# Optimization experiments

Hardware: AMD Instinct MI355X
Metric: run time of the kernel (lower is better)

The kernel has to match this reference:

```python
import jax, jax.numpy as jnp
import numpy as np
import math

B, H, W, CIN = 8, 64, 64, 192
INNER, K, N, P = 384, 2, 32, 64
NHK = INNER // P          # heads per scan direction = 6
NH = K * NHK              # total heads = 12
HID = 4 * CIN

def _silu(v):
    return v * jax.nn.sigmoid(v)

def setup_inputs() -> dict:
    key = jax.random.key(0)
    ks = jax.random.split(key, 12)
    x = jax.random.normal(ks[0], (B, H, W, CIN), jnp.float32)
    W_in = jax.random.normal(ks[1], (2 * INNER, CIN), jnp.float32) * 0.02
    conv_w = jax.random.normal(ks[2], (INNER, 1, 3, 3), jnp.float32) * 0.1
    conv_b = jnp.zeros((INNER,), jnp.float32)
    x_proj_weight = jax.random.normal(ks[3], (K, 2 * N + NHK, INNER), jnp.float32) * 0.02
    A_logs = jnp.log(jax.random.uniform(ks[4], (NH,), jnp.float32, 1.0, 16.0))
    Ds = jnp.ones((NH,), jnp.float32)
    u = jax.random.uniform(ks[5], (NH,), jnp.float32)
    dt = jnp.exp(u * (math.log(0.1) - math.log(0.001)) + math.log(0.001))
    dt = jnp.clip(dt, 1e-4, None)
    dt_bias = dt + jnp.log(-jnp.expm1(-dt))
    init_states = jnp.zeros((NH, P, N), jnp.float32)
    W_out = jax.random.normal(ks[6], (CIN, INNER), jnp.float32) * 0.02
    W1 = jax.random.normal(ks[7], (HID, CIN), jnp.float32) * 0.02
    b1 = jnp.zeros((HID,), jnp.float32)
    W2 = jax.random.normal(ks[8], (CIN, HID), jnp.float32) * 0.02
    b2 = jnp.zeros((CIN,), jnp.float32)
    return dict(x=x, W_in=W_in, conv_w=conv_w, conv_b=conv_b, x_proj_weight=x_proj_weight,
                A_logs=A_logs, Ds=Ds, dt_bias=dt_bias, init_states=init_states,
                W_out=W_out, W1=W1, b1=b1, W2=W2, b2=b2)

def reference(x, W_in, conv_w, conv_b, x_proj_weight, A_logs, Ds, dt_bias,
              init_states, W_out, W1, b1, W2, b2):
    Bb, Hh, Ww, Cin = x.shape
    L = Hh * Ww
    inner = W_in.shape[0] // 2
    shortcut = x
    # norm1 is identity (norm=None). in_proj (no bias), split into x and gate z
    xz = jnp.einsum('bhwc,dc->bhwd', x, W_in)
    xl, z = jnp.split(xz, 2, axis=-1)
    # depthwise conv (NCHW) + SiLU
    xc = jnp.transpose(xl, (0, 3, 1, 2))
    xc = jax.lax.conv_general_dilated(xc, conv_w, (1, 1), 'SAME',
                                      feature_group_count=inner,
                                      dimension_numbers=('NCHW', 'OIHW', 'NCHW'))
    xc = _silu(xc + conv_b[None, :, None, None])
    # cross scan: row-major and transposed (W-major) flattenings
    xs = jnp.stack([xc.reshape(Bb, inner, L),
                    jnp.transpose(xc, (0, 1, 3, 2)).reshape(Bb, inner, L)], axis=1)  # (B,K,inner,L)
    # project to B, C, dt per direction
    BCdt = jnp.einsum('bkdl,kcd->blkc', xs, x_proj_weight)  # (B,L,K,2N+NHK)
    Bs = BCdt[..., :N]                     # (B,L,K,N)
    Cs = BCdt[..., N:2 * N]                # (B,L,K,N)
    dt = BCdt[..., 2 * N:].reshape(Bb, L, NH)
    xh = jnp.transpose(xs, (0, 3, 1, 2)).reshape(Bb, L, NH, P)  # heads: k-major
    # Mamba2 selective scan (dt_softplus with bias)
    dt = jax.nn.softplus(dt + dt_bias)     # (B,L,NH)
    A = -jnp.exp(A_logs)                   # (NH,)
    da = jnp.exp(dt * A)                   # (B,L,NH)
    dtx = dt[..., None] * xh               # (B,L,NH,P)
    Bh = jnp.repeat(Bs, NHK, axis=2)       # (B,L,NH,N) group -> heads
    Ch = jnp.repeat(Cs, NHK, axis=2)
    h0 = jnp.broadcast_to(init_states, (Bb,) + init_states.shape)  # (B,NH,P,N)
    def step(h, inp):
        da_t, dtx_t, B_t, C_t = inp
        h = da_t[..., None, None] * h + dtx_t[..., None] * B_t[:, :, None, :]
        y_t = jnp.einsum('bhpn,bhn->bhp', h, C_t)
        return h, y_t
    _, ys = jax.lax.scan(step, h0, (jnp.moveaxis(da, 1, 0), jnp.moveaxis(dtx, 1, 0),
                                    jnp.moveaxis(Bh, 1, 0), jnp.moveaxis(Ch, 1, 0)))
    y = jnp.moveaxis(ys, 0, 1) + Ds[None, None, :, None] * xh  # (B,L,NH,P)
    out_y = jnp.transpose(y.reshape(Bb, L, K, inner), (0, 2, 3, 1))  # (B,K,inner,L)
    # scan_proj: undo each direction's flattening and sum
    y0 = out_y[:, 0].reshape(Bb, inner, Hh, Ww)
    y1 = jnp.transpose(out_y[:, 1].reshape(Bb, inner, Ww, Hh), (0, 1, 3, 2))
    yr = jnp.transpose((y0 + y1).reshape(Bb, inner, L), (0, 2, 1)).reshape(Bb, Hh, Ww, inner)
    # gate, out_proj, residual, MLP branch (dense is identity since in==out)
    yg = yr * _silu(z)
    out = shortcut + jnp.einsum('bhwd,cd->bhwc', yg, W_out)
    h1 = _silu(jnp.einsum('...c,dc->...d', out, W1) + b1)
    mlp = jnp.einsum('...d,cd->...c', h1, W2) + b2
    return out + mlp
```

## Files before the change

### kernel.cpp

```cpp
#include <hip/hip_runtime.h>
#include <math.h>

#define BB 8
#define HH 64
#define WW 64
#define CIN 192
#define INNER 384
#define LL 4096
#define NSTATE 32
#define PDIM 64
#define NHK 6
#define NHEADS 12
#define HID 768
#define CPROJ 70
#define QC 64
#define NC 64

#define WS_XLZ   0u
#define WS_XC    50331648u
#define WS_Y1    75497472u
#define WS_BCBF  100663296u
#define WS_DTRAW 109051904u
#define WS_DTV   119013376u
#define WS_CUMS  120586240u
#define WS_SHB   122159104u
#define WS_Y0    147324928u
#define WS_XBF   172490752u
#define WS_WINB  185073664u
#define WS_WPADB 185368576u
#define WS_WOUTB 185565184u
#define WS_W1B   185761792u
#define WS_W2B   186056704u
#define WS_REQ   186449920u

typedef __attribute__((ext_vector_type(8))) short short8;
typedef __attribute__((ext_vector_type(4))) float f32x4;

__device__ __forceinline__ float silu_f(float x) { return x / (1.f + __expf(-x)); }

__device__ __forceinline__ unsigned short f2bf(float f) {
    unsigned u = __float_as_uint(f);
    u += 0x7fffu + ((u >> 16) & 1u);
    return (unsigned short)(u >> 16);
}
__device__ __forceinline__ float bf2f(unsigned short u) {
    return __uint_as_float(((unsigned)u) << 16);
}

template<int EPI, int TRANSA>
__global__ __launch_bounds__(256)
void gemm_bf16(const unsigned short* __restrict__ A, const unsigned short* __restrict__ Wt,
               const float* __restrict__ bias, const float* __restrict__ res,
               float* __restrict__ Cf, unsigned short* __restrict__ Cb,
               int Kd, int ldc, int nmax)
{
    __shared__ __align__(16) short Als[128 * 64];
    __shared__ __align__(16) short Bls[128 * 64];
    const int tid = threadIdx.x;
    const int m0 = blockIdx.x * 128;
    const int n0 = blockIdx.y * 128;
    const int lane = tid & 63;
    const int wv = tid >> 6;
    const int wm = (wv >> 1) << 6;
    const int wn = (wv & 1) << 6;

    const unsigned short* gA[4];
    const unsigned short* gB[4];
    int lw[4];
    #pragma unroll
    for (int c = 0; c < 4; ++c) {
        const int idx = c * 256 + tid;
        const int row = idx >> 3;
        const int kb  = idx & 7;
        const int sb  = kb ^ (row & 7);
        lw[c] = row * 64 + sb * 8;
        size_t arow;
        const int mm = m0 + row;
        if (TRANSA) {
            const int bq = mm >> 12, lq = mm & 4095;
            arow = ((size_t)bq << 12) + (size_t)(((lq & 63) << 6) + (lq >> 6));
        } else {
            arow = (size_t)mm;
        }
        gA[c] = A + arow * Kd + kb * 8;
        gB[c] = Wt + (size_t)(n0 + row) * Kd + kb * 8;
    }

    f32x4 acc[4][4];
    #pragma unroll
    for (int i = 0; i < 4; ++i)
        #pragma unroll
        for (int j = 0; j < 4; ++j) acc[i][j] = (f32x4){0.f, 0.f, 0.f, 0.f};

    const int NT = Kd >> 6;
    short8 pA[4], pB[4];
    #pragma unroll
    for (int c = 0; c < 4; ++c) {
        pA[c] = *(const short8*)(gA[c]);
        pB[c] = *(const short8*)(gB[c]);
    }
    for (int kt = 0; kt < NT; ++kt) {
        __syncthreads();
        #pragma unroll
        for (int c = 0; c < 4; ++c) {
            *(short8*)&Als[lw[c]] = pA[c];
            *(short8*)&Bls[lw[c]] = pB[c];
        }
        __syncthreads();
        if (kt + 1 < NT) {
            #pragma unroll
            for (int c = 0; c < 4; ++c) {
                pA[c] = *(const short8*)(gA[c] + (kt + 1) * 64);
                pB[c] = *(const short8*)(gB[c] + (kt + 1) * 64);
            }
        }
        #pragma unroll
        for (int ks = 0; ks < 2; ++ks) {
            short8 af[4], bfr[4];
            #pragma unroll
            for (int r = 0; r < 4; ++r) {
                const int rowa = wm + r * 16 + (lane & 15);
                const int rowb = wn + r * 16 + (lane & 15);
                const int kb = ks * 4 + (lane >> 4);
                af[r]  = *(const short8*)&Als[rowa * 64 + ((kb ^ (rowa & 7)) << 3)];
                bfr[r] = *(const short8*)&Bls[rowb * 64 + ((kb ^ (rowb & 7)) << 3)];
            }
            #pragma unroll
            for (int mr = 0; mr < 4; ++mr)
                #pragma unroll
                for (int nr = 0; nr < 4; ++nr)
                    acc[mr][nr] = __builtin_amdgcn_mfma_f32_16x16x32_bf16(af[mr], bfr[nr], acc[mr][nr], 0, 0, 0);
        }
    }
    #pragma unroll
    for (int mr = 0; mr < 4; ++mr) {
        #pragma unroll
        for (int nr = 0; nr < 4; ++nr) {
            const int n = n0 + wn + nr * 16 + (lane & 15);
            if (n >= nmax) continue;
            const int mb = m0 + wm + mr * 16 + ((lane >> 4) << 2);
            #pragma unroll
            for (int q = 0; q < 4; ++q) {
                const size_t off = (size_t)(mb + q) * ldc + n;
                float v = acc[mr][nr][q];
                if (EPI == 0) { Cf[off] = v; }
                else if (EPI == 1) { v = silu_f(v + bias[n]); Cb[off] = f2bf(v); }
                else if (EPI == 2) { v += bias[n] + res[off]; Cf[off] = v; }
                else if (EPI == 3) { v += res[off]; Cf[off] = v; Cb[off] = f2bf(v); }
                else if (EPI == 4) { Cb[off] = f2bf(v); }
                else if (EPI == 5) {
                    if (n < 64) Cb[(size_t)(mb + q) * 128 + n] = f2bf(v);
                    else        Cf[(size_t)(mb + q) * 12 + (n - 64)] = v;
                }
            }
        }
    }
}

__global__ __launch_bounds__(256)
void cvt_kernel(const float* __restrict__ src, unsigned short* __restrict__ dst, int n)
{
    const int i = blockIdx.x * 256 + threadIdx.x;
    if (i < n) dst[i] = f2bf(src[i]);
}

__global__ __launch_bounds__(256)
void cvt_pad_kernel(const float* __restrict__ src, unsigned short* __restrict__ dst,
                    int srcRows, int total, int cols)
{
    const int i = blockIdx.x * 256 + threadIdx.x;
    if (i >= total) return;
    const int r = i / cols;
    dst[i] = (r < srcRows) ? f2bf(src[i]) : (unsigned short)0;
}

__global__ __launch_bounds__(256)
void conv_dw_kernel(const unsigned short* __restrict__ xlz, const float* __restrict__ cw,
                    const float* __restrict__ cb, unsigned short* __restrict__ xcbf)
{
    const int t = blockIdx.x * 256 + threadIdx.x;
    const int dv = t % (INNER / 8);
    const int m  = t / (INNER / 8);
    const int b = m >> 12;
    const int r = m & 4095;
    const int i = r >> 6;
    const int j = r & 63;
    const int d0 = dv * 8;

    float wreg[72];
    {
        const float4* w4 = (const float4*)(cw + d0 * 9);
        #pragma unroll
        for (int u = 0; u < 18; ++u) {
            const float4 v = w4[u];
            wreg[4*u+0] = v.x; wreg[4*u+1] = v.y; wreg[4*u+2] = v.z; wreg[4*u+3] = v.w;
        }
    }
    float acc[8];
    {
        const float4 b0 = *(const float4*)(cb + d0);
        const float4 b1 = *(const float4*)(cb + d0 + 4);
        acc[0]=b0.x; acc[1]=b0.y; acc[2]=b0.z; acc[3]=b0.w;
        acc[4]=b1.x; acc[5]=b1.y; acc[6]=b1.z; acc[7]=b1.w;
    }
    #pragma unroll
    for (int di = 0; di < 3; ++di) {
        const int ii = i + di - 1;
        if (ii < 0 || ii >= HH) continue;
        #pragma unroll
        for (int dj = 0; dj < 3; ++dj) {
            const int jj = j + dj - 1;
            if (jj < 0 || jj >= WW) continue;
            const uint4 v = *(const uint4*)(xlz + (((size_t)b << 12) + (size_t)(ii * 64 + jj)) * 768 + d0);
            const int t9 = di * 3 + dj;
            const unsigned ua[4] = {v.x, v.y, v.z, v.w};
            #pragma unroll
            for (int w2 = 0; w2 < 4; ++w2) {
                const float xlo = __uint_as_float(ua[w2] << 16);
                const float xhi = __uint_as_float(ua[w2] & 0xffff0000u);
                acc[2*w2+0] = fmaf(xlo, wreg[(2*w2+0)*9 + t9], acc[2*w2+0]);
                acc[2*w2+1] = fmaf(xhi, wreg[(2*w2+1)*9 + t9], acc[2*w2+1]);
            }
        }
    }
    unsigned o[4];
    #pragma unroll
    for (int w2 = 0; w2 < 4; ++w2) {
        const unsigned lo = f2bf(silu_f(acc[2*w2+0]));
        const unsigned hi = f2bf(silu_f(acc[2*w2+1]));
        o[w2] = lo | (hi << 16);
    }
    *(uint4*)(xcbf + (size_t)m * INNER + d0) = make_uint4(o[0], o[1], o[2], o[3]);
}

__global__ __launch_bounds__(256)
void dtcums_kernel(const float* __restrict__ dtraw, const float* __restrict__ dt_bias,
                   const float* __restrict__ A_logs,
                   float* __restrict__ dtv, float* __restrict__ cums)
{
    const int w = blockIdx.x * 4 + (threadIdx.x >> 6);
    const int lane = threadIdx.x & 63;
    const int b = w / (NHEADS * NC);
    const int rem = w - b * (NHEADS * NC);
    const int h = rem / NC;
    const int c = rem - h * NC;
    const int k = h / NHK;
    const int hq = h - k * NHK;
    const int l = c * QC + lane;
    const float dtr = dtraw[(((size_t)b * LL + l) * 2 + k) * 6 + hq];
    const float xx = dtr + dt_bias[h];
    const float sp = (xx > 20.f) ? xx : log1pf(expf(xx));
    float s = -expf(A_logs[h]) * sp;
    #pragma unroll
    for (int d = 1; d < 64; d <<= 1) {
        const float o = __shfl_up(s, d);
        if (lane >= d) s += o;
    }
    dtv[((size_t)b * LL + l) * NHEADS + h] = sp;
    cums[((size_t)b * LL + l) * NHEADS + h] = s;
}

__global__ __launch_bounds__(256)
void chunk_state_kernel(const unsigned short* __restrict__ xcbf, const unsigned short* __restrict__ BCbf,
                        const float* __restrict__ dtv, const float* __restrict__ cums,
                        unsigned short* __restrict__ SHb)
{
    __shared__ __align__(16) unsigned short Xb[PDIM][72];
    __shared__ __align__(16) unsigned short Bsc[NSTATE][72];
    __shared__ float cuS[QC], rs[QC];
    const int c = blockIdx.x, h = blockIdx.y, b = blockIdx.z;
    const int k = h / NHK;
    const int dch0 = (h - k * NHK) * PDIM;
    const int tid = threadIdx.x;
    const int lane = tid & 63;
    const int w = tid >> 6;

    #pragma unroll
    for (int r = 0; r < 16; ++r) {
        const int idx = tid + r * 256;
        const int m = idx >> 6, p = idx & 63;
        const int pos = (k == 0) ? (c * QC + m) : (m * QC + c);
        Xb[p][m] = xcbf[(((size_t)b << 12) + pos) * INNER + dch0 + p];
    }
    if (tid < QC)
        cuS[tid] = cums[((size_t)b * LL + c * QC + tid) * NHEADS + h];
    __syncthreads();
    if (tid < QC)
        rs[tid] = dtv[((size_t)b * LL + c * QC + tid) * NHEADS + h] * __expf(cuS[QC-1] - cuS[tid]);
    __syncthreads();
    #pragma unroll
    for (int r = 0; r < 8; ++r) {
        const int idx = tid + r * 256;
        const int m = idx >> 5, n = idx & 31;
        Bsc[n][m] = f2bf(rs[m] * bf2f(BCbf[(((size_t)b * LL + c * QC + m) * 2 + k) * 64 + n]));
    }
    __syncthreads();

    const int rowf = lane & 15;
    const int ko   = lane >> 4;
    f32x4 acc[2] = {{0.f,0.f,0.f,0.f},{0.f,0.f,0.f,0.f}};
    #pragma unroll
    for (int ks = 0; ks < 2; ++ks) {
        const short8 af = *(const short8*)&Xb[w * 16 + rowf][ks * 32 + ko * 8];
        #pragma unroll
        for (int nt = 0; nt < 2; ++nt) {
            const short8 bfr = *(const short8*)&Bsc[nt * 16 + rowf][ks * 32 + ko * 8];
            acc[nt] = __builtin_amdgcn_mfma_f32_16x16x32_bf16(af, bfr, acc[nt], 0, 0, 0);
        }
    }
    unsigned short* base = SHb + ((((size_t)b * NHEADS + h) * NC + c) * PDIM) * NSTATE;
    #pragma unroll
    for (int nt = 0; nt < 2; ++nt) {
        #pragma unroll
        for (int q = 0; q < 4; ++q) {
            const int p = w * 16 + ko * 4 + q;
            base[p * NSTATE + nt * 16 + rowf] = f2bf(acc[nt][q]);
        }
    }
}

__global__ __launch_bounds__(64)
void state_scan_kernel(unsigned short* __restrict__ SHb, const float* __restrict__ cums,
                       const float* __restrict__ init_states)
{
    __shared__ float decays[NC];
    const int g = blockIdx.x;
    const int bh = g >> 2;
    const int quarter = g & 3;
    const int b = bh / NHEADS;
    const int h = bh % NHEADS;
    const int tid = threadIdx.x;
    decays[tid] = __expf(cums[((size_t)b * LL + tid * QC + QC - 1) * NHEADS + h]);
    __syncthreads();
    const int p = quarter * 16 + (tid >> 2);
    const int nb = (tid & 3) * 8;
    float hs[8];
    {
        const float* is = init_states + ((size_t)h * PDIM + p) * NSTATE + nb;
        #pragma unroll
        for (int i = 0; i < 8; ++i) hs[i] = is[i];
    }
    unsigned short* base = SHb + (((size_t)b * NHEADS + h) * NC) * (PDIM * NSTATE) + p * NSTATE + nb;
    for (int c = 0; c < NC; ++c) {
        unsigned short* slot = base + (size_t)c * (PDIM * NSTATE);
        const uint4 sv = *(const uint4*)slot;
        const unsigned ua[4] = {sv.x, sv.y, sv.z, sv.w};
        unsigned o[4];
        #pragma unroll
        for (int w2 = 0; w2 < 4; ++w2)
            o[w2] = (unsigned)f2bf(hs[2*w2]) | ((unsigned)f2bf(hs[2*w2+1]) << 16);
        *(uint4*)slot = make_uint4(o[0], o[1], o[2], o[3]);
        const float dc = decays[c];
        #pragma unroll
        for (int w2 = 0; w2 < 4; ++w2) {
            hs[2*w2+0] = fmaf(dc, hs[2*w2+0], __uint_as_float(ua[w2] << 16));
            hs[2*w2+1] = fmaf(dc, hs[2*w2+1], __uint_as_float(ua[w2] & 0xffff0000u));
        }
    }
}

__global__ __launch_bounds__(256)
void intra_kernel(const unsigned short* __restrict__ xcbf, const unsigned short* __restrict__ BCbf,
                  const float* __restrict__ dtv, const float* __restrict__ cums,
                  const unsigned short* __restrict__ SHb, const float* __restrict__ Ds,
                  unsigned short* __restrict__ y0, unsigned short* __restrict__ y1)
{
    __shared__ __align__(16) unsigned short Bs[QC][40];
    __shared__ __align__(16) unsigned short Cs[QC][40];
    __shared__ __align__(16) unsigned short Hs[PDIM][40];
    __shared__ __align__(16) unsigned short Xb[PDIM][72];
    __shared__ __align__(16) unsigned short Gb[QC][72];
    __shared__ float cuS[QC], dtS[QC], Ei[QC];
    const int c = blockIdx.x, h = blockIdx.y, b = blockIdx.z;
    const int k = h / NHK;
    const int dch0 = (h - k * NHK) * PDIM;
    const int tid = threadIdx.x;
    const int lane = tid & 63;
    const int w = tid >> 6;

    #pragma unroll
    for (int r = 0; r < 16; ++r) {
        const int idx = tid + r * 256;
        const int m = idx >> 6, p = idx & 63;
        const int pos = (k == 0) ? (c * QC + m) : (m * QC + c);
        Xb[p][m] = xcbf[(((size_t)b << 12) + pos) * INNER + dch0 + p];
    }
    #pragma unroll
    for (int r = 0; r < 2; ++r) {
        const int idx = tid + r * 256;
        const int i = idx >> 3, ch = idx & 7;
        const uint4 v = *(const uint4*)(BCbf + (((size_t)b * LL + c * QC + i) * 2 + k) * 64 + ch * 8);
        if (ch < 4) *(uint4*)&Bs[i][ch * 8] = v;
        else        *(uint4*)&Cs[i][(ch - 4) * 8] = v;
    }
    {
        const int p = tid >> 2, ch = tid & 3;
        *(uint4*)&Hs[p][ch * 8] =
            *(const uint4*)(SHb + ((((size_t)b * NHEADS + h) * NC + c) * PDIM + p) * NSTATE + ch * 8);
    }
    if (tid < QC) {
        const size_t o = ((size_t)b * LL + c * QC + tid) * NHEADS + h;
        const float cu = cums[o];
        cuS[tid] = cu;
        dtS[tid] = dtv[o];
        Ei[tid]  = __expf(cu);
    }
    __syncthreads();

    const int rowf = lane & 15;
    const int ko   = lane >> 4;
    const short8 cfrag = *(const short8*)&Cs[w * 16 + rowf][ko * 8];

    f32x4 graw[4];
    #pragma unroll
    for (int mt = 0; mt < 4; ++mt) {
        const short8 bfrag = *(const short8*)&Bs[mt * 16 + rowf][ko * 8];
        graw[mt] = __builtin_amdgcn_mfma_f32_16x16x32_bf16(cfrag, bfrag, (f32x4){0.f,0.f,0.f,0.f}, 0, 0, 0);
    }
    #pragma unroll
    for (int mt = 0; mt < 4; ++mt) {
        const int m = mt * 16 + rowf;
        const float cum = cuS[m];
        const float dtm = dtS[m];
        #pragma unroll
        for (int q = 0; q < 4; ++q) {
            const int i = w * 16 + ko * 4 + q;
            float g = 0.f;
            if (m <= i) g = __expf(fminf(cuS[i] - cum, 0.f)) * dtm * graw[mt][q];
            Gb[i][m] = f2bf(g);
        }
    }
    f32x4 acc[4];
    #pragma unroll
    for (int pt = 0; pt < 4; ++pt) {
        const short8 hfrag = *(const short8*)&Hs[pt * 16 + rowf][ko * 8];
        acc[pt] = __builtin_amdgcn_mfma_f32_16x16x32_bf16(cfrag, hfrag, (f32x4){0.f,0.f,0.f,0.f}, 0, 0, 0);
    }
    const float Dh = Ds[h];
    #pragma unroll
    for (int pt = 0; pt < 4; ++pt) {
        const int p = pt * 16 + rowf;
        #pragma unroll
        for (int q = 0; q < 4; ++q) {
            const int i = w * 16 + ko * 4 + q;
            acc[pt][q] = acc[pt][q] * Ei[i] + Dh * bf2f(Xb[p][i]);
        }
    }
    #pragma unroll
    for (int ks = 0; ks < 2; ++ks) {
        const short8 gfrag = *(const short8*)&Gb[w * 16 + rowf][ks * 32 + ko * 8];
        #pragma unroll
        for (int pt = 0; pt < 4; ++pt) {
            const short8 xfrag = *(const short8*)&Xb[pt * 16 + rowf][ks * 32 + ko * 8];
            acc[pt] = __builtin_amdgcn_mfma_f32_16x16x32_bf16(gfrag, xfrag, acc[pt], 0, 0, 0);
        }
    }
    unsigned short* yk = (k == 0) ? y0 : y1;
    #pragma unroll
    for (int pt = 0; pt < 4; ++pt) {
        const int p = pt * 16 + rowf;
        #pragma unroll
        for (int q = 0; q < 4; ++q) {
            const int i = w * 16 + ko * 4 + q;
            const int pos = (k == 0) ? (c * QC + i) : (i * QC + c);
            yk[(((size_t)b << 12) + pos) * INNER + dch0 + p] = f2bf(acc[pt][q]);
        }
    }
}

__global__ __launch_bounds__(256)
void gate_kernel(const unsigned short* __restrict__ y0, const unsigned short* __restrict__ y1,
                 const unsigned short* __restrict__ xlz, unsigned short* __restrict__ ygbf)
{
    const int t = blockIdx.x * 256 + threadIdx.x;
    const int dv = t % (INNER / 8);
    const int m  = t / (INNER / 8);
    const int d0 = dv * 8;
    const uint4 a = *(const uint4*)(y0 + (size_t)m * INNER + d0);
    const uint4 bv = *(const uint4*)(y1 + (size_t)m * INNER + d0);
    const uint4 zv = *(const uint4*)(xlz + (size_t)m * 768 + INNER + d0);
    const unsigned ua[4] = {a.x, a.y, a.z, a.w};
    const unsigned ub[4] = {bv.x, bv.y, bv.z, bv.w};
    const unsigned uz[4] = {zv.x, zv.y, zv.z, zv.w};
    unsigned o[4];
    #pragma unroll
    for (int w2 = 0; w2 < 4; ++w2) {
        const float ylo = __uint_as_float(ua[w2] << 16) + __uint_as_float(ub[w2] << 16);
        const float yhi = __uint_as_float(ua[w2] & 0xffff0000u) + __uint_as_float(ub[w2] & 0xffff0000u);
        const float zlo = __uint_as_float(uz[w2] << 16);
        const float zhi = __uint_as_float(uz[w2] & 0xffff0000u);
        o[w2] = (unsigned)f2bf(ylo * silu_f(zlo)) | ((unsigned)f2bf(yhi * silu_f(zhi)) << 16);
    }
    *(uint4*)(ygbf + (size_t)m * INNER + d0) = make_uint4(o[0], o[1], o[2], o[3]);
}

__global__ __launch_bounds__(256)
void report_ws_kernel(float* __restrict__ out, int n, float val)
{
    const int e = blockIdx.x * 256 + threadIdx.x;
    if (e < n) out[e] = val;
}

extern "C" void kernel_launch(void* const* d_in, const int* in_sizes, int n_in,
                              void* d_out, int out_size, void* d_ws, size_t ws_size,
                              hipStream_t stream)
{
    const float* x          = (const float*)d_in[0];
    const float* W_in       = (const float*)d_in[1];
    const float* conv_w     = (const float*)d_in[2];
    const float* conv_b     = (const float*)d_in[3];
    const float* xpw        = (const float*)d_in[4];
    const float* A_logs     = (const float*)d_in[5];
    const float* Ds         = (const float*)d_in[6];
    const float* dt_bias    = (const float*)d_in[7];
    const float* init_states= (const float*)d_in[8];
    const float* W_out      = (const float*)d_in[9];
    const float* W1         = (const float*)d_in[10];
    const float* b1         = (const float*)d_in[11];
    const float* W2         = (const float*)d_in[12];
    const float* b2         = (const float*)d_in[13];
    float* out = (float*)d_out;

    if (ws_size < (size_t)WS_REQ) {
        const float mib = (float)((double)ws_size / 1048576.0);
        report_ws_kernel<<<(out_size + 255) / 256, 256, 0, stream>>>(out, out_size, mib);
        return;
    }

    char* ws = (char*)d_ws;
    unsigned short* xlz   = (unsigned short*)(ws + WS_XLZ);
    unsigned short* xc_bf = (unsigned short*)(ws + WS_XC);
    unsigned short* y1    = (unsigned short*)(ws + WS_Y1);
    unsigned short* BCbf  = (unsigned short*)(ws + WS_BCBF);
    float* dtraw = (float*)(ws + WS_DTRAW);
    float* dtv   = (float*)(ws + WS_DTV);
    float* cums  = (float*)(ws + WS_CUMS);
    unsigned short* SHb   = (unsigned short*)(ws + WS_SHB);
    unsigned short* y0    = (unsigned short*)(ws + WS_Y0);
    unsigned short* x_bf  = (unsigned short*)(ws + WS_XBF);
    unsigned short* Winb  = (unsigned short*)(ws + WS_WINB);
    unsigned short* wpadb = (unsigned short*)(ws + WS_WPADB);
    unsigned short* Woutb = (unsigned short*)(ws + WS_WOUTB);
    unsigned short* W1b   = (unsigned short*)(ws + WS_W1B);
    unsigned short* W2b   = (unsigned short*)(ws + WS_W2B);
    unsigned short* yg_bf  = (unsigned short*)(ws + WS_XC);
    unsigned short* out_bf = (unsigned short*)(ws + WS_BCBF);
    unsigned short* h1_bf  = (unsigned short*)(ws + WS_XLZ);

    const int M = BB * LL;

    cvt_kernel<<<(M * CIN + 255) / 256, 256, 0, stream>>>(x, x_bf, M * CIN);
    cvt_kernel<<<(HID * CIN + 255) / 256, 256, 0, stream>>>(W_in, Winb, HID * CIN);
    cvt_kernel<<<(HID * CIN + 255) / 256, 256, 0, stream>>>(W1, W1b, HID * CIN);
    cvt_pad_kernel<<<(128 * INNER + 255) / 256, 256, 0, stream>>>(xpw, wpadb, CPROJ, 128 * INNER, INNER);
    cvt_pad_kernel<<<(128 * INNER + 255) / 256, 256, 0, stream>>>(xpw + CPROJ * INNER, wpadb + 128 * INNER, CPROJ, 128 * INNER, INNER);
    cvt_pad_kernel<<<(256 * INNER + 255) / 256, 256, 0, stream>>>(W_out, Woutb, CIN, 256 * INNER, INNER);
    cvt_pad_kernel<<<(256 * HID + 255) / 256, 256, 0, stream>>>(W2, W2b, CIN, 256 * HID, HID);

    gemm_bf16<4,0><<<dim3(M/128, HID/128), 256, 0, stream>>>(x_bf, Winb, nullptr, nullptr, nullptr, xlz, CIN, HID, HID);

    conv_dw_kernel<<<(M * INNER / 8) / 256, 256, 0, stream>>>(xlz, conv_w, conv_b, xc_bf);

    gemm_bf16<5,0><<<dim3(M/128, 1), 256, 0, stream>>>(xc_bf, wpadb, nullptr, nullptr, dtraw, BCbf, INNER, 0, CPROJ);
    gemm_bf16<5,1><<<dim3(M/128, 1), 256, 0, stream>>>(xc_bf, wpadb + 128 * INNER, nullptr, nullptr, dtraw + 6, BCbf + 64, INNER, 0, CPROJ);

    dtcums_kernel<<<(BB * NHEADS * NC) / 4, 256, 0, stream>>>(dtraw, dt_bias, A_logs, dtv, cums);

    chunk_state_kernel<<<dim3(NC, NHEADS, BB), 256, 0, stream>>>(xc_bf, BCbf, dtv, cums, SHb);
    state_scan_kernel<<<BB * NHEADS * 4, 64, 0, stream>>>(SHb, cums, init_states);
    intra_kernel<<<dim3(NC, NHEADS, BB), 256, 0, stream>>>(xc_bf, BCbf, dtv, cums, SHb, Ds, y0, y1);

    gate_kernel<<<(M * INNER / 8) / 256, 256, 0, stream>>>(y0, y1, xlz, yg_bf);

    gemm_bf16<3,0><<<dim3(M/128, 2), 256, 0, stream>>>(yg_bf, Woutb, nullptr, x, out, out_bf, INNER, CIN, CIN);

    gemm_bf16<1,0><<<dim3(M/128, HID/128), 256, 0, stream>>>(out_bf, W1b, b1, nullptr, nullptr, h1_bf, CIN, HID, HID);
    gemm_bf16<2,0><<<dim3(M/128, 2), 256, 0, stream>>>(h1_bf, W2b, b2, out, out, nullptr, HID, CIN, CIN);
}
```

Baseline: 275.9 us.

## Merge weight conversions into one kernel and reuse rows in depthwise conv

Six separate weight-conversion launches are replaced by a single kernel that branches on flat index, cutting launch overhead. The depthwise 3x3 conv now has each thread compute 8 vertically consecutive output pixels, keeping a sliding window of three input rows in registers. Each new output row then needs 3 loads instead of 9. The trade-offs are higher register pressure and 8x fewer threads, which lowers available parallelism.

```diff
diff --git a/kernel.cpp b/kernel.cpp
--- a/kernel.cpp
+++ b/kernel.cpp
@@ -165,13 +165,36 @@
 }
 
 __global__ __launch_bounds__(256)
-void cvt_pad_kernel(const float* __restrict__ src, unsigned short* __restrict__ dst,
-                    int srcRows, int total, int cols)
-{
-    const int i = blockIdx.x * 256 + threadIdx.x;
-    if (i >= total) return;
-    const int r = i / cols;
-    dst[i] = (r < srcRows) ? f2bf(src[i]) : (unsigned short)0;
+void cvt_weights_kernel(const float* __restrict__ W_in, const float* __restrict__ W1,
+                        const float* __restrict__ xpw, const float* __restrict__ W_out,
+                        const float* __restrict__ W2,
+                        unsigned short* __restrict__ Winb, unsigned short* __restrict__ W1b,
+                        unsigned short* __restrict__ wpadb, unsigned short* __restrict__ Woutb,
+                        unsigned short* __restrict__ W2b)
+{
+    int i = blockIdx.x * 256 + threadIdx.x;
+    if (i < 147456) { Winb[i] = f2bf(W_in[i]); return; }
+    i -= 147456;
+    if (i < 147456) { W1b[i] = f2bf(W1[i]); return; }
+    i -= 147456;
+    if (i < 98304) {
+        const int d = i % 384;
+        const int rr = (i / 384) & 127;
+        const int k = i / 49152;
+        wpadb[i] = (rr < CPROJ) ? f2bf(xpw[((size_t)k * CPROJ + rr) * 384 + d]) : (unsigned short)0;
+        return;
+    }
+    i -= 98304;
+    if (i < 98304) {
+        const int rr = i / 384;
+        Woutb[i] = (rr < CIN) ? f2bf(W_out[i]) : (unsigned short)0;
+        return;
+    }
+    i -= 98304;
+    if (i < 196608) {
+        const int rr = i / 768;
+        W2b[i] = (rr < CIN) ? f2bf(W2[i]) : (unsigned short)0;
+    }
 }
 
 __global__ __launch_bounds__(256)
@@ -179,13 +202,13 @@
                     const float* __restrict__ cb, unsigned short* __restrict__ xcbf)
 {
     const int t = blockIdx.x * 256 + threadIdx.x;
-    const int dv = t % (INNER / 8);
-    const int m  = t / (INNER / 8);
-    const int b = m >> 12;
-    const int r = m & 4095;
-    const int i = r >> 6;
-    const int j = r & 63;
+    const int dv = t % 48;
+    int r = t / 48;
+    const int j  = r & 63;  r >>= 6;
+    const int ib = r & 7;   r >>= 3;
+    const int b  = r;
     const int d0 = dv * 8;
+    const int i0 = ib * 8;
 
     float wreg[72];
     {
@@ -193,44 +216,74 @@
         #pragma unroll
         for (int u = 0; u < 18; ++u) {
             const float4 v = w4[u];
-            wreg[4*u+0] = v.x; wreg[4*u+1] = v.y; wreg[4*u+2] = v.z; wreg[4*u+3] = v.w;
-        }
-    }
-    float acc[8];
+            wreg[4*u+0]=v.x; wreg[4*u+1]=v.y; wreg[4*u+2]=v.z; wreg[4*u+3]=v.w;
+        }
+    }
+    float bias[8];
     {
         const float4 b0 = *(const float4*)(cb + d0);
         const float4 b1 = *(const float4*)(cb + d0 + 4);
-        acc[0]=b0.x; acc[1]=b0.y; acc[2]=b0.z; acc[3]=b0.w;
-        acc[4]=b1.x; acc[5]=b1.y; acc[6]=b1.z; acc[7]=b1.w;
-    }
-    #pragma unroll
-    for (int di = 0; di < 3; ++di) {
-        const int ii = i + di - 1;
-        if (ii < 0 || ii >= HH) continue;
-        #pragma unroll
-        for (int dj = 0; dj < 3; ++dj) {
-            const int jj = j + dj - 1;
-            if (jj < 0 || jj >= WW) continue;
-            const uint4 v = *(const uint4*)(xlz + (((size_t)b << 12) + (size_t)(ii * 64 + jj)) * 768 + d0);
-            const int t9 = di * 3 + dj;
-            const unsigned ua[4] = {v.x, v.y, v.z, v.w};
+        bias[0]=b0.x; bias[1]=b0.y; bias[2]=b0.z; bias[3]=b0.w;
+        bias[4]=b1.x; bias[5]=b1.y; bias[6]=b1.z; bias[7]=b1.w;
+    }
+
+    const unsigned short* base = xlz + ((size_t)b << 12) * 768 + d0;
+    const int jok[3] = { (j - 1 >= 0), 1, (j + 1 < WW) };
+
+    unsigned rm[3][4], r0[3][4], rp[3][4];
+    #pragma unroll
+    for (int cj = 0; cj < 3; ++cj) {
+        uint4 vm = make_uint4(0,0,0,0), v0 = make_uint4(0,0,0,0);
+        if (jok[cj]) {
+            if (i0 - 1 >= 0) vm = *(const uint4*)(base + (size_t)((i0-1) * 64 + j - 1 + cj) * 768);
+            v0 = *(const uint4*)(base + (size_t)(i0 * 64 + j - 1 + cj) * 768);
+        }
+        rm[cj][0]=vm.x; rm[cj][1]=vm.y; rm[cj][2]=vm.z; rm[cj][3]=vm.w;
+        r0[cj][0]=v0.x; r0[cj][1]=v0.y; r0[cj][2]=v0.z; r0[cj][3]=v0.w;
+    }
+
+    #pragma unroll
+    for (int ii = 0; ii < 8; ++ii) {
+        const int i = i0 + ii;
+        #pragma unroll
+        for (int cj = 0; cj < 3; ++cj) {
+            uint4 vp = make_uint4(0,0,0,0);
+            if (jok[cj] && (i + 1 < HH))
+                vp = *(const uint4*)(base + (size_t)((i+1) * 64 + j - 1 + cj) * 768);
+            rp[cj][0]=vp.x; rp[cj][1]=vp.y; rp[cj][2]=vp.z; rp[cj][3]=vp.w;
+        }
+        float acc[8];
+        #pragma unroll
+        for (int ch = 0; ch < 8; ++ch) acc[ch] = bias[ch];
+        #pragma unroll
+        for (int cj = 0; cj < 3; ++cj) {
             #pragma unroll
             for (int w2 = 0; w2 < 4; ++w2) {
-                const float xlo = __uint_as_float(ua[w2] << 16);
-                const float xhi = __uint_as_float(ua[w2] & 0xffff0000u);
-                acc[2*w2+0] = fmaf(xlo, wreg[(2*w2+0)*9 + t9], acc[2*w2+0]);
-                acc[2*w2+1] = fmaf(xhi, wreg[(2*w2+1)*9 + t9], acc[2*w2+1]);
+                acc[2*w2+0] = fmaf(__uint_as_float(rm[cj][w2] << 16),        wreg[(2*w2+0)*9 + cj],     acc[2*w2+0]);
+                acc[2*w2+1] = fmaf(__uint_as_float(rm[cj][w2] & 0xffff0000u), wreg[(2*w2+1)*9 + cj],     acc[2*w2+1]);
+                acc[2*w2+0] = fmaf(__uint_as_float(r0[cj][w2] << 16),        wreg[(2*w2+0)*9 + 3 + cj], acc[2*w2+0]);
+                acc[2*w2+1] = fmaf(__uint_as_float(r0[cj][w2] & 0xffff0000u), wreg[(2*w2+1)*9 + 3 + cj], acc[2*w2+1]);
+                acc[2*w2+0] = fmaf(__uint_as_float(rp[cj][w2] << 16),        wreg[(2*w2+0)*9 + 6 + cj], acc[2*w2+0]);
+                acc[2*w2+1] = fmaf(__uint_as_float(rp[cj][w2] & 0xffff0000u), wreg[(2*w2+1)*9 + 6 + cj], acc[2*w2+1]);
             }
         }
-    }
-    unsigned o[4];
-    #pragma unroll
-    for (int w2 = 0; w2 < 4; ++w2) {
-        const unsigned lo = f2bf(silu_f(acc[2*w2+0]));
-        const unsigned hi = f2bf(silu_f(acc[2*w2+1]));
-        o[w2] = lo | (hi << 16);
-    }
-    *(uint4*)(xcbf + (size_t)m * INNER + d0) = make_uint4(o[0], o[1], o[2], o[3]);
+        unsigned o[4];
+        #pragma unroll
+        for (int w2 = 0; w2 < 4; ++w2) {
+            const unsigned lo = f2bf(silu_f(acc[2*w2+0]));
+            const unsigned hi = f2bf(silu_f(acc[2*w2+1]));
+            o[w2] = lo | (hi << 16);
+        }
+        *(uint4*)(xcbf + ((size_t)(b << 12) + (size_t)(i * 64 + j)) * INNER + d0) =
+            make_uint4(o[0], o[1], o[2], o[3]);
+        #pragma unroll
+        for (int cj = 0; cj < 3; ++cj)
+            #pragma unroll
+            for (int w2 = 0; w2 < 4; ++w2) {
+                rm[cj][w2] = r0[cj][w2];
+                r0[cj][w2] = rp[cj][w2];
+            }
+    }
 }
 
 __global__ __launch_bounds__(256)
@@ -550,16 +603,12 @@
     const int M = BB * LL;
 
     cvt_kernel<<<(M * CIN + 255) / 256, 256, 0, stream>>>(x, x_bf, M * CIN);
-    cvt_kernel<<<(HID * CIN + 255) / 256, 256, 0, stream>>>(W_in, Winb, HID * CIN);
-    cvt_kernel<<<(HID * CIN + 255) / 256, 256, 0, stream>>>(W1, W1b, HID * CIN);
-    cvt_pad_kernel<<<(128 * INNER + 255) / 256, 256, 0, stream>>>(xpw, wpadb, CPROJ, 128 * INNER, INNER);
-    cvt_pad_kernel<<<(128 * INNER + 255) / 256, 256, 0, stream>>>(xpw + CPROJ * INNER, wpadb + 128 * INNER, CPROJ, 128 * INNER, INNER);
-    cvt_pad_kernel<<<(256 * INNER + 255) / 256, 256, 0, stream>>>(W_out, Woutb, CIN, 256 * INNER, INNER);
-    cvt_pad_kernel<<<(256 * HID + 255) / 256, 256, 0, stream>>>(W2, W2b, CIN, 256 * HID, HID);
+    cvt_weights_kernel<<<(688128 + 255) / 256, 256, 0, stream>>>(W_in, W1, xpw, W_out, W2,
+                                                                 Winb, W1b, wpadb, Woutb, W2b);
 
     gemm_bf16<4,0><<<dim3(M/128, HID/128), 256, 0, stream>>>(x_bf, Winb, nullptr, nullptr, nullptr, xlz, CIN, HID, HID);
 
-    conv_dw_kernel<<<(M * INNER / 8) / 256, 256, 0, stream>>>(xlz, conv_w, conv_b, xc_bf);
+    conv_dw_kernel<<<196608 / 256, 256, 0, stream>>>(xlz, conv_w, conv_b, xc_bf);
 
     gemm_bf16<5,0><<<dim3(M/128, 1), 256, 0, stream>>>(xc_bf, wpadb, nullptr, nullptr, dtraw, BCbf, INNER, 0, CPROJ);
     gemm_bf16<5,1><<<dim3(M/128, 1), 256, 0, stream>>>(xc_bf, wpadb + 128 * INNER, nullptr, nullptr, dtraw + 6, BCbf + 64, INNER, 0, CPROJ);
```

Result: faster. 241.7 us (-12.4%).
